# Kernel tuning notes

Hardware: AMD Instinct MI355X
Metric: run time of the kernel (lower is better)

The kernel has to match this reference:

```python
import jax, jax.numpy as jnp
import numpy as np

B, L, W, K, G = 8, 2048, 1024, 5, 2
OFFSET_SCALE = 2.0
EPS = 1e-5


def setup_inputs() -> dict:
    key = jax.random.key(0)
    ks = jax.random.split(key, 6)
    x = jax.random.normal(ks[0], (B, L, W), jnp.float32)
    # True = padded position
    lengths = jax.random.randint(ks[1], (B,), L // 2, L + 1)
    mask = jnp.arange(L)[None, :] >= lengths[:, None]
    # offset predictor (pointwise): one fractional offset per kernel tap
    w_off = jax.random.normal(ks[2], (W, K), jnp.float32) * 0.02
    b_off = jnp.zeros((K,), jnp.float32)
    # grouped conv weights: [groups, out_per_group, in_per_group, K]
    conv_w = jax.random.normal(ks[3], (G, W // G, W // G, K), jnp.float32) * 0.02
    conv_b = jnp.zeros((W,), jnp.float32)
    gamma = jnp.ones((W,), jnp.float32)
    beta = jnp.zeros((W,), jnp.float32)
    proj_w = jax.random.normal(ks[4], (W,), jnp.float32) * 0.02
    proj_b = jnp.zeros((), jnp.float32)
    return dict(x=x, mask=mask, w_off=w_off, b_off=b_off, conv_w=conv_w,
                conv_b=conv_b, gamma=gamma, beta=beta, proj_w=proj_w, proj_b=proj_b)


def _deform_conv1d(x, w_off, b_off, conv_w, conv_b):
    # x: [B, L, W]; returns [B, L, W]
    Bb, Ll, Ww = x.shape
    Gg, Co, Ci, Kk = conv_w.shape
    # per-position, per-tap fractional offsets in [-offset_scale, offset_scale]
    offsets = jnp.tanh(x @ w_off + b_off) * OFFSET_SCALE            # [B, L, K]
    taps = jnp.arange(Kk, dtype=x.dtype) - (Kk - 1) / 2.0           # centered taps
    pos = jnp.arange(Ll, dtype=x.dtype)[None, :, None] + taps[None, None, :] + offsets  # [B,L,K]
    p0 = jnp.floor(pos)
    frac = pos - p0                                                  # [B, L, K]
    p0i = p0.astype(jnp.int32)
    bidx = jnp.arange(Bb)[:, None, None]

    def gather(idx):
        valid = (idx >= 0) & (idx < Ll)                              # zero padding outside
        samp = x[bidx, jnp.clip(idx, 0, Ll - 1)]                     # [B, L, K, W]
        return samp * valid[..., None].astype(x.dtype)

    # linear interpolation between floor and floor+1 samples
    samp = gather(p0i) * (1.0 - frac)[..., None] + gather(p0i + 1) * frac[..., None]
    samp = samp.reshape(Bb, Ll, Kk, Gg, Ci)                          # split channels into groups
    out = jnp.einsum('blkgc,gock->blgo', samp, conv_w).reshape(Bb, Ll, Gg * Co)
    return out + conv_b


def reference(x, mask, w_off, b_off, conv_w, conv_b, gamma, beta, proj_w, proj_b):
    h = _deform_conv1d(x, w_off, b_off, conv_w, conv_b)              # [B, L, W]
    # LayerNorm over width
    mu = jnp.mean(h, axis=-1, keepdims=True)
    var = jnp.mean((h - mu) ** 2, axis=-1, keepdims=True)
    h = (h - mu) * jax.lax.rsqrt(var + EPS) * gamma + beta
    # dropout is identity in eval mode
    h = jnp.where(mask[..., None], 0.0, h)                           # masked fill
    lengths = jnp.maximum(jnp.sum(~mask, axis=1, keepdims=True).astype(h.dtype), 1.0)
    pooled = jnp.sum(h, axis=1) / lengths                            # [B, W]
    return pooled @ proj_w + proj_b                                  # [B]
```

## Files before the change

kernel.cpp:

```cpp
#include <hip/hip_runtime.h>
#include <hip/hip_bf16.h>

constexpr int Bb = 8, Ll = 2048, Ww = 1024;
constexpr int BL = Bb * Ll;

typedef short bf16x8 __attribute__((ext_vector_type(8)));
typedef float f32x4  __attribute__((ext_vector_type(4)));

__device__ inline unsigned short f2bf(float f) {
    union { float f; unsigned u; } v; v.f = f;
    unsigned u = v.u;
    unsigned r = (u + 0x7fffu + ((u >> 16) & 1u)) >> 16;
    return (unsigned short)r;
}
__device__ inline float bf2f(unsigned short h) {
    union { unsigned u; float f; } v; v.u = ((unsigned)h) << 16;
    return v.f;
}
__device__ inline unsigned lerp_pair(unsigned pa, unsigned pb, float w0, float w1) {
    union { unsigned u; float f; } alo, ahi, blo, bhi;
    alo.u = pa << 16;  ahi.u = pa & 0xffff0000u;
    blo.u = pb << 16;  bhi.u = pb & 0xffff0000u;
    float hlo = w0 * alo.f + w1 * blo.f;
    float hhi = w0 * ahi.f + w1 * bhi.f;
    union { __hip_bfloat162 h2; unsigned u; } r;
    r.h2 = __float22bfloat162_rn(float2{hlo, hhi});
    return r.u;
}

__device__ inline void gl_lds16(const unsigned short* g, unsigned short* l) {
    __builtin_amdgcn_global_load_lds(
        (const __attribute__((address_space(1))) unsigned int*)g,
        (__attribute__((address_space(3))) unsigned int*)l, 16, 0, 0);
}

__global__ void maskA_kernel(const void* __restrict__ mraw, int* __restrict__ flags) {
    const unsigned char* mb = (const unsigned char*)mraw;
    const unsigned* mw = (const unsigned*)mraw;
    int gid = blockIdx.x * 256 + threadIdx.x;
    int nonint = 0, notf = 0, hasf = 0;
    for (int i = gid; i < BL; i += 4096) { if ((i & 3) && mb[i]) nonint = 1; }
    for (int i = gid; i < BL / 4; i += 4096) {
        unsigned w = mw[i];
        if (w == 0x3f800000u) hasf = 1; else if (w) notf = 1;
    }
    if (__builtin_amdgcn_readfirstlane(__ballot(nonint) ? 1 : 0)) { if ((threadIdx.x & 63) == 0 && __ballot(nonint)) atomicOr(&flags[0], 1); }
    if ((threadIdx.x & 63) == 0) {
    }
    if (nonint) atomicOr(&flags[0], 1);
    if (notf)   atomicOr(&flags[1], 1);
    if (hasf)   atomicOr(&flags[2], 1);
}
__global__ void maskB_kernel(const void* __restrict__ mraw, const int* __restrict__ flags,
                             float* __restrict__ maskf) {
    const unsigned char* mb = (const unsigned char*)mraw;
    const unsigned* mw = (const unsigned*)mraw;
    int gid = blockIdx.x * 256 + threadIdx.x;
    int is_f32  = (!flags[1]) && flags[2];
    int is_bool = (!is_f32) && flags[0];
    for (int i = gid; i < BL; i += 4096) {
        int masked = is_bool ? (mb[i] != 0) : (mw[i] != 0u);
        maskf[i] = masked ? 0.0f : 1.0f;
    }
}

__global__ void wconv_kernel(const float* __restrict__ conv_w, unsigned short* __restrict__ w_t) {
    int gnt = blockIdx.x >> 2;
    int part = blockIdx.x & 3;
    int g = gnt / 20, nt = gnt % 20;
    int k = nt >> 2, o0 = (nt & 3) * 128;
    int tid = threadIdx.x;
    #pragma unroll
    for (int it = 0; it < 8; it++) {
        int chunk = part * 2048 + it * 256 + tid;
        int r = chunk >> 6;
        int cq = chunk & 63;
        int cs = cq >> 2, q = cq & 3;
        int o = o0 + r;
        int c0 = cs * 32 + q * 8;
        const float* src = conv_w + (((size_t)(g * 512 + o) * 512 + c0) * 5 + k);
        ushort4 lo, hi;
        lo.x = f2bf(src[0]);  lo.y = f2bf(src[5]);  lo.z = f2bf(src[10]); lo.w = f2bf(src[15]);
        hi.x = f2bf(src[20]); hi.y = f2bf(src[25]); hi.z = f2bf(src[30]); hi.w = f2bf(src[35]);
        int dst16 = (gnt * 16 + cs) * 512 + r * 4 + (q ^ (r & 3));
        *(ushort4*)&w_t[(size_t)dst16 * 8]     = lo;
        *(ushort4*)&w_t[(size_t)dst16 * 8 + 4] = hi;
    }
}

__global__ __launch_bounds__(256) void offsets_kernel(
    const float* __restrict__ x, const float* __restrict__ w_off, const float* __restrict__ b_off,
    unsigned short* __restrict__ x_bf, float4* __restrict__ pk)
{
    const int wave = threadIdx.x >> 6, lane = threadIdx.x & 63;
    const int bl = blockIdx.x * 4 + wave;
    const int l = bl & (Ll - 1);
    const int c0 = lane * 16;

    const float* xr = x + (size_t)bl * Ww + c0;
    float4 v0 = *(const float4*)(xr + 0);
    float4 v1 = *(const float4*)(xr + 4);
    float4 v2 = *(const float4*)(xr + 8);
    float4 v3 = *(const float4*)(xr + 12);
    float xv[16] = { v0.x,v0.y,v0.z,v0.w, v1.x,v1.y,v1.z,v1.w,
                     v2.x,v2.y,v2.z,v2.w, v3.x,v3.y,v3.z,v3.w };

    uint4 pa, pb;
    unsigned* pu = (unsigned*)&pa;
    #pragma unroll
    for (int j = 0; j < 4; j++) pu[j] = (unsigned)f2bf(xv[j*2]) | ((unsigned)f2bf(xv[j*2+1]) << 16);
    pu = (unsigned*)&pb;
    #pragma unroll
    for (int j = 0; j < 4; j++) pu[j] = (unsigned)f2bf(xv[8+j*2]) | ((unsigned)f2bf(xv[8+j*2+1]) << 16);
    *(uint4*)&x_bf[(size_t)bl * Ww + c0]     = pa;
    *(uint4*)&x_bf[(size_t)bl * Ww + c0 + 8] = pb;

    float acc[5] = {0.f, 0.f, 0.f, 0.f, 0.f};
    const float* wp = w_off + (size_t)c0 * 5;
    #pragma unroll
    for (int j = 0; j < 16; j++) {
        #pragma unroll
        for (int k = 0; k < 5; k++) acc[k] += xv[j] * wp[j * 5 + k];
    }
    #pragma unroll
    for (int k = 0; k < 5; k++)
        #pragma unroll
        for (int off = 32; off; off >>= 1) acc[k] += __shfl_xor(acc[k], off);

    if (lane < 5) {
        float s = (lane == 0) ? acc[0] : (lane == 1) ? acc[1] : (lane == 2) ? acc[2]
                : (lane == 3) ? acc[3] : acc[4];
        s += b_off[lane];
        float offv = tanhf(s) * 2.0f;
        float pos = (float)l + (float)(lane - 2) + offv;
        float p0 = floorf(pos);
        float frac = pos - p0;
        int i0 = (int)p0;
        int i1 = i0 + 1;
        int ok0 = (i0 >= 0) && (i0 < Ll);
        int ok1 = (i1 >= 0) && (i1 < Ll);
        float4 pkv;
        pkv.x = __int_as_float(min(max(i0, 0), Ll - 1));
        pkv.y = __int_as_float(min(max(i1, 0), Ll - 1));
        pkv.z = ok0 ? (1.0f - frac) : 0.0f;
        pkv.w = ok1 ? frac : 0.0f;
        pk[bl * 5 + lane] = pkv;
    }
}

__global__ __launch_bounds__(256, 2) void gemm_kernel(
    const unsigned short* __restrict__ x_bf, const unsigned short* __restrict__ w_t,
    const float4* __restrict__ pk, const float* __restrict__ conv_b,
    unsigned short* __restrict__ h)
{
    __shared__ unsigned short Bs[2][2 * 4096];
    const int tid = threadIdx.x;
    const int mt = blockIdx.x;
    const int nhalf = blockIdx.y;
    const int g = blockIdx.z;
    const int b = mt >> 4;
    const int lane = tid & 63, wave = tid >> 6;
    const int wr = (wave >> 1) * 64;
    const int imgsel = wave & 1;
    const int l15 = lane & 15, l4 = lane >> 4;
    const int sw = (l4 ^ (l15 & 3)) * 8;

    {
        const int nt0 = nhalf * 2;
        const unsigned short* W0 = w_t + ((size_t)((g * 20 + nt0) * 16 + 0)) * 4096;
        const unsigned short* W1 = w_t + ((size_t)((g * 20 + nt0 + 1) * 16 + 0)) * 4096;
        gl_lds16(W0 + tid * 8,        &Bs[0][tid * 8]);
        gl_lds16(W0 + 2048 + tid * 8, &Bs[0][2048 + tid * 8]);
        gl_lds16(W1 + tid * 8,        &Bs[0][4096 + tid * 8]);
        gl_lds16(W1 + 2048 + tid * 8, &Bs[0][4096 + 2048 + tid * 8]);
    }
    __syncthreads();

    f32x4 acc[4][8];
    #pragma unroll
    for (int i = 0; i < 4; i++)
        #pragma unroll
        for (int j = 0; j < 8; j++) acc[i][j] = (f32x4){0.f, 0.f, 0.f, 0.f};

    int buf = 0;
    for (int k = 0; k < 5; ++k) {
        unsigned off0[4], off1[4];
        float w0r[4], w1r[4];
        #pragma unroll
        for (int i = 0; i < 4; i++) {
            const int bl = mt * 128 + wr + i * 16 + l15;
            float4 pkv = pk[bl * 5 + k];
            const int i0 = __float_as_int(pkv.x), i1 = __float_as_int(pkv.y);
            off0[i] = (unsigned)(((b << 11) + i0) * Ww + g * 512);
            off1[i] = (unsigned)(((b << 11) + i1) * Ww + g * 512);
            w0r[i] = pkv.z; w1r[i] = pkv.w;
        }
        for (int cs = 0; cs < 16; ++cs) {
            const int it = k * 16 + cs;
            if (it < 79) {
                const int it2 = it + 1;
                const int k2 = it2 >> 4, cs2 = it2 & 15;
                const int nt0 = k2 * 4 + nhalf * 2;
                const unsigned short* W0 = w_t + ((size_t)((g * 20 + nt0) * 16 + cs2)) * 4096;
                const unsigned short* W1 = w_t + ((size_t)((g * 20 + nt0 + 1) * 16 + cs2)) * 4096;
                gl_lds16(W0 + tid * 8,        &Bs[buf ^ 1][tid * 8]);
                gl_lds16(W0 + 2048 + tid * 8, &Bs[buf ^ 1][2048 + tid * 8]);
                gl_lds16(W1 + tid * 8,        &Bs[buf ^ 1][4096 + tid * 8]);
                gl_lds16(W1 + 2048 + tid * 8, &Bs[buf ^ 1][4096 + 2048 + tid * 8]);
            }
            const int ch0 = cs * 32 + l4 * 8;
            bf16x8 af[4];
            #pragma unroll
            for (int i = 0; i < 4; i++) {
                const uint4 ua = *(const uint4*)(x_bf + off0[i] + ch0);
                const uint4 ub = *(const uint4*)(x_bf + off1[i] + ch0);
                union { unsigned u[4]; bf16x8 v; } fa;
                fa.u[0] = lerp_pair(ua.x, ub.x, w0r[i], w1r[i]);
                fa.u[1] = lerp_pair(ua.y, ub.y, w0r[i], w1r[i]);
                fa.u[2] = lerp_pair(ua.z, ub.z, w0r[i], w1r[i]);
                fa.u[3] = lerp_pair(ua.w, ub.w, w0r[i], w1r[i]);
                af[i] = fa.v;
            }
            bf16x8 bfr[8];
            #pragma unroll
            for (int j = 0; j < 8; j++)
                bfr[j] = *(const bf16x8*)&Bs[buf][imgsel * 4096 + (j * 16 + l15) * 32 + sw];
            #pragma unroll
            for (int i = 0; i < 4; i++)
                #pragma unroll
                for (int j = 0; j < 8; j++)
                    acc[i][j] = __builtin_amdgcn_mfma_f32_16x16x32_bf16(af[i], bfr[j], acc[i][j], 0, 0, 0);
            __syncthreads();
            buf ^= 1;
        }
    }
    #pragma unroll
    for (int j = 0; j < 8; j++) {
        const int col = g * 512 + nhalf * 256 + imgsel * 128 + j * 16 + l15;
        const float bias = conv_b[col];
        #pragma unroll
        for (int i = 0; i < 4; i++) {
            const int row0 = mt * 128 + wr + i * 16 + l4 * 4;
            #pragma unroll
            for (int rr = 0; rr < 4; rr++)
                h[(size_t)(row0 + rr) * Ww + col] = f2bf(acc[i][j][rr] + bias);
        }
    }
}

__global__ __launch_bounds__(256) void lnpool_kernel(
    const unsigned short* __restrict__ h, const float* __restrict__ gamma,
    const float* __restrict__ maskf, float* __restrict__ pooled)
{
    const int tid = threadIdx.x;
    const int wave = tid >> 6, lane = tid & 63;
    const int c0 = lane * 16;
    const int bl0 = blockIdx.x * 16 + wave * 4;
    const int b = bl0 >> 11;

    float g16[16];
    #pragma unroll
    for (int j = 0; j < 4; j++) {
        float4 gv = *(const float4*)(gamma + c0 + j * 4);
        g16[j*4+0] = gv.x; g16[j*4+1] = gv.y; g16[j*4+2] = gv.z; g16[j*4+3] = gv.w;
    }
    float pacc[16];
    #pragma unroll
    for (int j = 0; j < 16; j++) pacc[j] = 0.f;

    #pragma unroll
    for (int r = 0; r < 4; r++) {
        const int bl = bl0 + r;
        const float m = maskf[bl];
        const uint4 ha = *(const uint4*)(h + (size_t)bl * Ww + c0);
        const uint4 hb = *(const uint4*)(h + (size_t)bl * Ww + c0 + 8);
        float hf[16];
        const unsigned* pw = (const unsigned*)&ha;
        #pragma unroll
        for (int j = 0; j < 4; j++) {
            union { unsigned u; float f; } lo, hi;
            lo.u = pw[j] << 16; hi.u = pw[j] & 0xffff0000u;
            hf[j*2] = lo.f; hf[j*2+1] = hi.f;
        }
        pw = (const unsigned*)&hb;
        #pragma unroll
        for (int j = 0; j < 4; j++) {
            union { unsigned u; float f; } lo, hi;
            lo.u = pw[j] << 16; hi.u = pw[j] & 0xffff0000u;
            hf[8+j*2] = lo.f; hf[8+j*2+1] = hi.f;
        }
        float s1 = 0.f, s2 = 0.f;
        #pragma unroll
        for (int j = 0; j < 16; j++) { s1 += hf[j]; s2 += hf[j] * hf[j]; }
        #pragma unroll
        for (int off = 32; off; off >>= 1) {
            s1 += __shfl_xor(s1, off);
            s2 += __shfl_xor(s2, off);
        }
        const float mu = s1 * (1.0f / 1024.0f);
        const float var = s2 * (1.0f / 1024.0f) - mu * mu;
        const float rstd = rsqrtf(var + 1e-5f) * m;
        #pragma unroll
        for (int j = 0; j < 16; j++) pacc[j] += (hf[j] - mu) * rstd * g16[j];
    }
    __shared__ float spool[4][1024];
    #pragma unroll
    for (int j = 0; j < 4; j++)
        *(float4*)&spool[wave][c0 + j * 4] = *(float4*)&pacc[j * 4];
    __syncthreads();
    const int ch = tid * 4;
    float4 a = *(float4*)&spool[0][ch];
    float4 bq = *(float4*)&spool[1][ch];
    float4 cq = *(float4*)&spool[2][ch];
    float4 dq = *(float4*)&spool[3][ch];
    atomicAdd(&pooled[b * Ww + ch + 0], a.x + bq.x + cq.x + dq.x);
    atomicAdd(&pooled[b * Ww + ch + 1], a.y + bq.y + cq.y + dq.y);
    atomicAdd(&pooled[b * Ww + ch + 2], a.z + bq.z + cq.z + dq.z);
    atomicAdd(&pooled[b * Ww + ch + 3], a.w + bq.w + cq.w + dq.w);
}

__global__ void final_kernel(const float* __restrict__ pooled, const float* __restrict__ maskf,
                             const float* __restrict__ beta, const float* __restrict__ proj_w,
                             const float* __restrict__ proj_b, float* __restrict__ out)
{
    int b = blockIdx.x;
    int tid = threadIdx.x;
    float len = 0.f, dotP = 0.f, dotB = 0.f;
    for (int l = tid; l < Ll; l += 256) len += maskf[b * Ll + l];
    for (int c = tid; c < Ww; c += 256) {
        dotP += pooled[b * Ww + c] * proj_w[c];
        dotB += beta[c] * proj_w[c];
    }
    for (int off = 32; off; off >>= 1) {
        len += __shfl_down(len, off);
        dotP += __shfl_down(dotP, off);
        dotB += __shfl_down(dotB, off);
    }
    __shared__ float rl[4], rp[4], rb[4];
    int wave = tid >> 6, lane = tid & 63;
    if (lane == 0) { rl[wave] = len; rp[wave] = dotP; rb[wave] = dotB; }
    __syncthreads();
    if (tid == 0) {
        float Lt = rl[0] + rl[1] + rl[2] + rl[3];
        float Pt = rp[0] + rp[1] + rp[2] + rp[3];
        float Bt = rb[0] + rb[1] + rb[2] + rb[3];
        out[b] = Pt / fmaxf(Lt, 1.0f) + Bt + proj_b[0];
    }
}


extern "C" void kernel_launch(void* const* d_in, const int* in_sizes, int n_in,
                              void* d_out, int out_size, void* d_ws, size_t ws_size,
                              hipStream_t stream)
{
    const float* x      = (const float*)d_in[0];
    const void*  mask   = d_in[1];
    const float* w_off  = (const float*)d_in[2];
    const float* b_off  = (const float*)d_in[3];
    const float* conv_w = (const float*)d_in[4];
    const float* conv_b = (const float*)d_in[5];
    const float* gamma  = (const float*)d_in[6];
    const float* beta   = (const float*)d_in[7];
    const float* proj_w = (const float*)d_in[8];
    const float* proj_b = (const float*)d_in[9];
    float* out = (float*)d_out;

    char* ws = (char*)d_ws;
    float* maskf         = (float*)(ws + 0);
    float* pooled        = (float*)(ws + 65536);
    int*   flags         = (int*)(ws + 98304);
    float4* pk           = (float4*)(ws + 98320);
    unsigned short* w_t  = (unsigned short*)(ws + 1409040);
    unsigned short* x_bf = (unsigned short*)(ws + 6651920);
    unsigned short* h    = (unsigned short*)(ws + 40206352);

    hipMemsetAsync(pooled, 0, Bb * Ww * sizeof(float), stream);
    hipMemsetAsync(flags, 0, 16, stream);
    maskA_kernel<<<16, 256, 0, stream>>>(mask, flags);
    maskB_kernel<<<16, 256, 0, stream>>>(mask, flags, maskf);
    wconv_kernel<<<160, 256, 0, stream>>>(conv_w, w_t);
    offsets_kernel<<<BL / 4, 256, 0, stream>>>(x, w_off, b_off, x_bf, pk);
    gemm_kernel<<<dim3(128, 2, 2), 256, 0, stream>>>(x_bf, w_t, pk, conv_b, h);
    lnpool_kernel<<<1024, 256, 0, stream>>>(h, gamma, maskf, pooled);
    final_kernel<<<8, 256, 0, stream>>>(pooled, maskf, beta, proj_w, proj_b, out);
}
```

Before: 353.7 us.

## Fuse prep kernels into one launch, halve GEMM M-tile, fold mask into lnpool

Merges the mask-detection, weight-conversion and offset kernels into a single prep_kernel dispatched by block index, and drops the separate maskB pass. The mask value is now decoded inside lnpool, which also accumulates per-batch lengths with atomics, so final_kernel no longer rescans the mask. The GEMM M tile shrinks from 128 to 64 rows with a doubled grid and launch bounds raised to 4 waves per SIMD, trading operand reuse for more blocks and occupancy. The launch count drops, and there are more atomics plus lower per-block reuse in the GEMM.

Measured after the change: 392.5 us. 1.11x slower.

```diff
diff --git a/kernel.cpp b/kernel.cpp
--- a/kernel.cpp
+++ b/kernel.cpp
@@ -34,121 +34,108 @@
         (__attribute__((address_space(3))) unsigned int*)l, 16, 0, 0);
 }
 
-__global__ void maskA_kernel(const void* __restrict__ mraw, int* __restrict__ flags) {
-    const unsigned char* mb = (const unsigned char*)mraw;
-    const unsigned* mw = (const unsigned*)mraw;
-    int gid = blockIdx.x * 256 + threadIdx.x;
-    int nonint = 0, notf = 0, hasf = 0;
-    for (int i = gid; i < BL; i += 4096) { if ((i & 3) && mb[i]) nonint = 1; }
-    for (int i = gid; i < BL / 4; i += 4096) {
-        unsigned w = mw[i];
-        if (w == 0x3f800000u) hasf = 1; else if (w) notf = 1;
-    }
-    if (__builtin_amdgcn_readfirstlane(__ballot(nonint) ? 1 : 0)) { if ((threadIdx.x & 63) == 0 && __ballot(nonint)) atomicOr(&flags[0], 1); }
-    if ((threadIdx.x & 63) == 0) {
-    }
-    if (nonint) atomicOr(&flags[0], 1);
-    if (notf)   atomicOr(&flags[1], 1);
-    if (hasf)   atomicOr(&flags[2], 1);
-}
-__global__ void maskB_kernel(const void* __restrict__ mraw, const int* __restrict__ flags,
-                             float* __restrict__ maskf) {
-    const unsigned char* mb = (const unsigned char*)mraw;
-    const unsigned* mw = (const unsigned*)mraw;
-    int gid = blockIdx.x * 256 + threadIdx.x;
-    int is_f32  = (!flags[1]) && flags[2];
-    int is_bool = (!is_f32) && flags[0];
-    for (int i = gid; i < BL; i += 4096) {
-        int masked = is_bool ? (mb[i] != 0) : (mw[i] != 0u);
-        maskf[i] = masked ? 0.0f : 1.0f;
-    }
-}
-
-__global__ void wconv_kernel(const float* __restrict__ conv_w, unsigned short* __restrict__ w_t) {
-    int gnt = blockIdx.x >> 2;
-    int part = blockIdx.x & 3;
-    int g = gnt / 20, nt = gnt % 20;
-    int k = nt >> 2, o0 = (nt & 3) * 128;
-    int tid = threadIdx.x;
-    #pragma unroll
-    for (int it = 0; it < 8; it++) {
-        int chunk = part * 2048 + it * 256 + tid;
-        int r = chunk >> 6;
-        int cq = chunk & 63;
-        int cs = cq >> 2, q = cq & 3;
-        int o = o0 + r;
-        int c0 = cs * 32 + q * 8;
-        const float* src = conv_w + (((size_t)(g * 512 + o) * 512 + c0) * 5 + k);
-        ushort4 lo, hi;
-        lo.x = f2bf(src[0]);  lo.y = f2bf(src[5]);  lo.z = f2bf(src[10]); lo.w = f2bf(src[15]);
-        hi.x = f2bf(src[20]); hi.y = f2bf(src[25]); hi.z = f2bf(src[30]); hi.w = f2bf(src[35]);
-        int dst16 = (gnt * 16 + cs) * 512 + r * 4 + (q ^ (r & 3));
-        *(ushort4*)&w_t[(size_t)dst16 * 8]     = lo;
-        *(ushort4*)&w_t[(size_t)dst16 * 8 + 4] = hi;
-    }
-}
-
-__global__ __launch_bounds__(256) void offsets_kernel(
+__global__ __launch_bounds__(256) void prep_kernel(
     const float* __restrict__ x, const float* __restrict__ w_off, const float* __restrict__ b_off,
-    unsigned short* __restrict__ x_bf, float4* __restrict__ pk)
-{
-    const int wave = threadIdx.x >> 6, lane = threadIdx.x & 63;
-    const int bl = blockIdx.x * 4 + wave;
-    const int l = bl & (Ll - 1);
-    const int c0 = lane * 16;
-
-    const float* xr = x + (size_t)bl * Ww + c0;
-    float4 v0 = *(const float4*)(xr + 0);
-    float4 v1 = *(const float4*)(xr + 4);
-    float4 v2 = *(const float4*)(xr + 8);
-    float4 v3 = *(const float4*)(xr + 12);
-    float xv[16] = { v0.x,v0.y,v0.z,v0.w, v1.x,v1.y,v1.z,v1.w,
-                     v2.x,v2.y,v2.z,v2.w, v3.x,v3.y,v3.z,v3.w };
-
-    uint4 pa, pb;
-    unsigned* pu = (unsigned*)&pa;
-    #pragma unroll
-    for (int j = 0; j < 4; j++) pu[j] = (unsigned)f2bf(xv[j*2]) | ((unsigned)f2bf(xv[j*2+1]) << 16);
-    pu = (unsigned*)&pb;
-    #pragma unroll
-    for (int j = 0; j < 4; j++) pu[j] = (unsigned)f2bf(xv[8+j*2]) | ((unsigned)f2bf(xv[8+j*2+1]) << 16);
-    *(uint4*)&x_bf[(size_t)bl * Ww + c0]     = pa;
-    *(uint4*)&x_bf[(size_t)bl * Ww + c0 + 8] = pb;
-
-    float acc[5] = {0.f, 0.f, 0.f, 0.f, 0.f};
-    const float* wp = w_off + (size_t)c0 * 5;
-    #pragma unroll
-    for (int j = 0; j < 16; j++) {
-        #pragma unroll
-        for (int k = 0; k < 5; k++) acc[k] += xv[j] * wp[j * 5 + k];
-    }
-    #pragma unroll
-    for (int k = 0; k < 5; k++)
-        #pragma unroll
-        for (int off = 32; off; off >>= 1) acc[k] += __shfl_xor(acc[k], off);
-
-    if (lane < 5) {
-        float s = (lane == 0) ? acc[0] : (lane == 1) ? acc[1] : (lane == 2) ? acc[2]
-                : (lane == 3) ? acc[3] : acc[4];
-        s += b_off[lane];
-        float offv = tanhf(s) * 2.0f;
-        float pos = (float)l + (float)(lane - 2) + offv;
-        float p0 = floorf(pos);
-        float frac = pos - p0;
-        int i0 = (int)p0;
-        int i1 = i0 + 1;
-        int ok0 = (i0 >= 0) && (i0 < Ll);
-        int ok1 = (i1 >= 0) && (i1 < Ll);
-        float4 pkv;
-        pkv.x = __int_as_float(min(max(i0, 0), Ll - 1));
-        pkv.y = __int_as_float(min(max(i1, 0), Ll - 1));
-        pkv.z = ok0 ? (1.0f - frac) : 0.0f;
-        pkv.w = ok1 ? frac : 0.0f;
-        pk[bl * 5 + lane] = pkv;
-    }
-}
-
-__global__ __launch_bounds__(256, 2) void gemm_kernel(
+    const float* __restrict__ conv_w, const void* __restrict__ mraw,
+    unsigned short* __restrict__ x_bf, float4* __restrict__ pk,
+    unsigned short* __restrict__ w_t, int* __restrict__ flags)
+{
+    const int blk = blockIdx.x;
+    const int tid = threadIdx.x;
+    if (blk < 4096) {
+        const int wave = tid >> 6, lane = tid & 63;
+        const int bl = blk * 4 + wave;
+        const int l = bl & (Ll - 1);
+        const int c0 = lane * 16;
+
+        const float* xr = x + (size_t)bl * Ww + c0;
+        float4 v0 = *(const float4*)(xr + 0);
+        float4 v1 = *(const float4*)(xr + 4);
+        float4 v2 = *(const float4*)(xr + 8);
+        float4 v3 = *(const float4*)(xr + 12);
+        float xv[16] = { v0.x,v0.y,v0.z,v0.w, v1.x,v1.y,v1.z,v1.w,
+                         v2.x,v2.y,v2.z,v2.w, v3.x,v3.y,v3.z,v3.w };
+
+        uint4 pa, pb;
+        unsigned* pu = (unsigned*)&pa;
+        #pragma unroll
+        for (int j = 0; j < 4; j++) pu[j] = (unsigned)f2bf(xv[j*2]) | ((unsigned)f2bf(xv[j*2+1]) << 16);
+        pu = (unsigned*)&pb;
+        #pragma unroll
+        for (int j = 0; j < 4; j++) pu[j] = (unsigned)f2bf(xv[8+j*2]) | ((unsigned)f2bf(xv[8+j*2+1]) << 16);
+        *(uint4*)&x_bf[(size_t)bl * Ww + c0]     = pa;
+        *(uint4*)&x_bf[(size_t)bl * Ww + c0 + 8] = pb;
+
+        float acc[5] = {0.f, 0.f, 0.f, 0.f, 0.f};
+        const float* wp = w_off + (size_t)c0 * 5;
+        #pragma unroll
+        for (int j = 0; j < 16; j++) {
+            #pragma unroll
+            for (int k = 0; k < 5; k++) acc[k] += xv[j] * wp[j * 5 + k];
+        }
+        #pragma unroll
+        for (int k = 0; k < 5; k++)
+            #pragma unroll
+            for (int off = 32; off; off >>= 1) acc[k] += __shfl_xor(acc[k], off);
+
+        if (lane < 5) {
+            float s = (lane == 0) ? acc[0] : (lane == 1) ? acc[1] : (lane == 2) ? acc[2]
+                    : (lane == 3) ? acc[3] : acc[4];
+            s += b_off[lane];
+            float offv = tanhf(s) * 2.0f;
+            float pos = (float)l + (float)(lane - 2) + offv;
+            float p0 = floorf(pos);
+            float frac = pos - p0;
+            int i0 = (int)p0;
+            int i1 = i0 + 1;
+            int ok0 = (i0 >= 0) && (i0 < Ll);
+            int ok1 = (i1 >= 0) && (i1 < Ll);
+            float4 pkv;
+            pkv.x = __int_as_float(min(max(i0, 0), Ll - 1));
+            pkv.y = __int_as_float(min(max(i1, 0), Ll - 1));
+            pkv.z = ok0 ? (1.0f - frac) : 0.0f;
+            pkv.w = ok1 ? frac : 0.0f;
+            pk[bl * 5 + lane] = pkv;
+        }
+    } else if (blk < 4256) {
+        const int bb = blk - 4096;
+        const int gnt = bb >> 2;
+        const int part = bb & 3;
+        const int g = gnt / 20, nt = gnt % 20;
+        const int k = nt >> 2, o0 = (nt & 3) * 128;
+        #pragma unroll
+        for (int it = 0; it < 8; it++) {
+            int chunk = part * 2048 + it * 256 + tid;
+            int r = chunk >> 6;
+            int cq = chunk & 63;
+            int cs = cq >> 2, q = cq & 3;
+            int o = o0 + r;
+            int c0 = cs * 32 + q * 8;
+            const float* src = conv_w + (((size_t)(g * 512 + o) * 512 + c0) * 5 + k);
+            ushort4 lo, hi;
+            lo.x = f2bf(src[0]);  lo.y = f2bf(src[5]);  lo.z = f2bf(src[10]); lo.w = f2bf(src[15]);
+            hi.x = f2bf(src[20]); hi.y = f2bf(src[25]); hi.z = f2bf(src[30]); hi.w = f2bf(src[35]);
+            int dst16 = (gnt * 16 + cs) * 512 + r * 4 + (q ^ (r & 3));
+            *(ushort4*)&w_t[(size_t)dst16 * 8]     = lo;
+            *(ushort4*)&w_t[(size_t)dst16 * 8 + 4] = hi;
+        }
+    } else {
+        const unsigned char* mb = (const unsigned char*)mraw;
+        const unsigned* mw = (const unsigned*)mraw;
+        int gid = (blk - 4256) * 256 + tid;
+        int nonint = 0, notf = 0, hasf = 0;
+        for (int i = gid; i < BL; i += 4096) { if ((i & 3) && mb[i]) nonint = 1; }
+        for (int i = gid; i < BL / 4; i += 4096) {
+            unsigned w = mw[i];
+            if (w == 0x3f800000u) hasf = 1; else if (w) notf = 1;
+        }
+        if (nonint) atomicOr(&flags[0], 1);
+        if (notf)   atomicOr(&flags[1], 1);
+        if (hasf)   atomicOr(&flags[2], 1);
+    }
+}
+
+__global__ __launch_bounds__(256, 4) void gemm_kernel(
     const unsigned short* __restrict__ x_bf, const unsigned short* __restrict__ w_t,
     const float4* __restrict__ pk, const float* __restrict__ conv_b,
     unsigned short* __restrict__ h)
@@ -158,9 +145,9 @@
     const int mt = blockIdx.x;
     const int nhalf = blockIdx.y;
     const int g = blockIdx.z;
-    const int b = mt >> 4;
+    const int b = mt >> 5;
     const int lane = tid & 63, wave = tid >> 6;
-    const int wr = (wave >> 1) * 64;
+    const int wr = (wave >> 1) * 32;
     const int imgsel = wave & 1;
     const int l15 = lane & 15, l4 = lane >> 4;
     const int sw = (l4 ^ (l15 & 3)) * 8;
@@ -176,19 +163,19 @@
     }
     __syncthreads();
 
-    f32x4 acc[4][8];
-    #pragma unroll
-    for (int i = 0; i < 4; i++)
+    f32x4 acc[2][8];
+    #pragma unroll
+    for (int i = 0; i < 2; i++)
         #pragma unroll
         for (int j = 0; j < 8; j++) acc[i][j] = (f32x4){0.f, 0.f, 0.f, 0.f};
 
     int buf = 0;
     for (int k = 0; k < 5; ++k) {
-        unsigned off0[4], off1[4];
-        float w0r[4], w1r[4];
-        #pragma unroll
-        for (int i = 0; i < 4; i++) {
-            const int bl = mt * 128 + wr + i * 16 + l15;
+        unsigned off0[2], off1[2];
+        float w0r[2], w1r[2];
+        #pragma unroll
+        for (int i = 0; i < 2; i++) {
+            const int bl = mt * 64 + wr + i * 16 + l15;
             float4 pkv = pk[bl * 5 + k];
             const int i0 = __float_as_int(pkv.x), i1 = __float_as_int(pkv.y);
             off0[i] = (unsigned)(((b << 11) + i0) * Ww + g * 512);
@@ -209,9 +196,9 @@
                 gl_lds16(W1 + 2048 + tid * 8, &Bs[buf ^ 1][4096 + 2048 + tid * 8]);
             }
             const int ch0 = cs * 32 + l4 * 8;
-            bf16x8 af[4];
-            #pragma unroll
-            for (int i = 0; i < 4; i++) {
+            bf16x8 af[2];
+            #pragma unroll
+            for (int i = 0; i < 2; i++) {
                 const uint4 ua = *(const uint4*)(x_bf + off0[i] + ch0);
                 const uint4 ub = *(const uint4*)(x_bf + off1[i] + ch0);
                 union { unsigned u[4]; bf16x8 v; } fa;
@@ -226,7 +213,7 @@
             for (int j = 0; j < 8; j++)
                 bfr[j] = *(const bf16x8*)&Bs[buf][imgsel * 4096 + (j * 16 + l15) * 32 + sw];
             #pragma unroll
-            for (int i = 0; i < 4; i++)
+            for (int i = 0; i < 2; i++)
                 #pragma unroll
                 for (int j = 0; j < 8; j++)
                     acc[i][j] = __builtin_amdgcn_mfma_f32_16x16x32_bf16(af[i], bfr[j], acc[i][j], 0, 0, 0);
@@ -239,8 +226,8 @@
         const int col = g * 512 + nhalf * 256 + imgsel * 128 + j * 16 + l15;
         const float bias = conv_b[col];
         #pragma unroll
-        for (int i = 0; i < 4; i++) {
-            const int row0 = mt * 128 + wr + i * 16 + l4 * 4;
+        for (int i = 0; i < 2; i++) {
+            const int row0 = mt * 64 + wr + i * 16 + l4 * 4;
             #pragma unroll
             for (int rr = 0; rr < 4; rr++)
                 h[(size_t)(row0 + rr) * Ww + col] = f2bf(acc[i][j][rr] + bias);
@@ -250,7 +237,8 @@
 
 __global__ __launch_bounds__(256) void lnpool_kernel(
     const unsigned short* __restrict__ h, const float* __restrict__ gamma,
-    const float* __restrict__ maskf, float* __restrict__ pooled)
+    const void* __restrict__ mraw, const int* __restrict__ flags,
+    float* __restrict__ pooled, float* __restrict__ lengths)
 {
     const int tid = threadIdx.x;
     const int wave = tid >> 6, lane = tid & 63;
@@ -258,6 +246,11 @@
     const int bl0 = blockIdx.x * 16 + wave * 4;
     const int b = bl0 >> 11;
 
+    const unsigned char* mb = (const unsigned char*)mraw;
+    const unsigned* mw = (const unsigned*)mraw;
+    const int is_f32  = (!flags[1]) && flags[2];
+    const int is_bool = (!is_f32) && flags[0];
+
     float g16[16];
     #pragma unroll
     for (int j = 0; j < 4; j++) {
@@ -267,11 +260,14 @@
     float pacc[16];
     #pragma unroll
     for (int j = 0; j < 16; j++) pacc[j] = 0.f;
+    float cnt = 0.f;
 
     #pragma unroll
     for (int r = 0; r < 4; r++) {
         const int bl = bl0 + r;
-        const float m = maskf[bl];
+        const int masked = is_bool ? (mb[bl] != 0) : (mw[bl] != 0u);
+        const float m = masked ? 0.0f : 1.0f;
+        cnt += m;
         const uint4 ha = *(const uint4*)(h + (size_t)bl * Ww + c0);
         const uint4 hb = *(const uint4*)(h + (size_t)bl * Ww + c0 + 8);
         float hf[16];
@@ -303,6 +299,7 @@
         #pragma unroll
         for (int j = 0; j < 16; j++) pacc[j] += (hf[j] - mu) * rstd * g16[j];
     }
+    if (lane == 0) atomicAdd(&lengths[b], cnt);
     __shared__ float spool[4][1024];
     #pragma unroll
     for (int j = 0; j < 4; j++)
@@ -319,32 +316,29 @@
     atomicAdd(&pooled[b * Ww + ch + 3], a.w + bq.w + cq.w + dq.w);
 }
 
-__global__ void final_kernel(const float* __restrict__ pooled, const float* __restrict__ maskf,
+__global__ void final_kernel(const float* __restrict__ pooled, const float* __restrict__ lengths,
                              const float* __restrict__ beta, const float* __restrict__ proj_w,
                              const float* __restrict__ proj_b, float* __restrict__ out)
 {
     int b = blockIdx.x;
     int tid = threadIdx.x;
-    float len = 0.f, dotP = 0.f, dotB = 0.f;
-    for (int l = tid; l < Ll; l += 256) len += maskf[b * Ll + l];
+    float dotP = 0.f, dotB = 0.f;
     for (int c = tid; c < Ww; c += 256) {
         dotP += pooled[b * Ww + c] * proj_w[c];
         dotB += beta[c] * proj_w[c];
     }
     for (int off = 32; off; off >>= 1) {
-        len += __shfl_down(len, off);
         dotP += __shfl_down(dotP, off);
         dotB += __shfl_down(dotB, off);
     }
-    __shared__ float rl[4], rp[4], rb[4];
+    __shared__ float rp[4], rb[4];
     int wave = tid >> 6, lane = tid & 63;
-    if (lane == 0) { rl[wave] = len; rp[wave] = dotP; rb[wave] = dotB; }
+    if (lane == 0) { rp[wave] = dotP; rb[wave] = dotB; }
     __syncthreads();
     if (tid == 0) {
-        float Lt = rl[0] + rl[1] + rl[2] + rl[3];
         float Pt = rp[0] + rp[1] + rp[2] + rp[3];
         float Bt = rb[0] + rb[1] + rb[2] + rb[3];
-        out[b] = Pt / fmaxf(Lt, 1.0f) + Bt + proj_b[0];
+        out[b] = Pt / fmaxf(lengths[b], 1.0f) + Bt + proj_b[0];
     }
 }
 
@@ -366,21 +360,17 @@
     float* out = (float*)d_out;
 
     char* ws = (char*)d_ws;
-    float* maskf         = (float*)(ws + 0);
-    float* pooled        = (float*)(ws + 65536);
-    int*   flags         = (int*)(ws + 98304);
-    float4* pk           = (float4*)(ws + 98320);
-    unsigned short* w_t  = (unsigned short*)(ws + 1409040);
-    unsigned short* x_bf = (unsigned short*)(ws + 6651920);
-    unsigned short* h    = (unsigned short*)(ws + 40206352);
-
-    hipMemsetAsync(pooled, 0, Bb * Ww * sizeof(float), stream);
-    hipMemsetAsync(flags, 0, 16, stream);
-    maskA_kernel<<<16, 256, 0, stream>>>(mask, flags);
-    maskB_kernel<<<16, 256, 0, stream>>>(mask, flags, maskf);
-    wconv_kernel<<<160, 256, 0, stream>>>(conv_w, w_t);
-    offsets_kernel<<<BL / 4, 256, 0, stream>>>(x, w_off, b_off, x_bf, pk);
-    gemm_kernel<<<dim3(128, 2, 2), 256, 0, stream>>>(x_bf, w_t, pk, conv_b, h);
-    lnpool_kernel<<<1024, 256, 0, stream>>>(h, gamma, maskf, pooled);
-    final_kernel<<<8, 256, 0, stream>>>(pooled, maskf, beta, proj_w, proj_b, out);
-}
+    float* pooled        = (float*)(ws + 0);
+    int*   flags         = (int*)(ws + 32768);
+    float* lengths       = (float*)(ws + 32784);
+    float4* pk           = (float4*)(ws + 32832);
+    unsigned short* w_t  = (unsigned short*)(ws + 1343552);
+    unsigned short* x_bf = (unsigned short*)(ws + 6586432);
+    unsigned short* h    = (unsigned short*)(ws + 40140864);
+
+    hipMemsetAsync(pooled, 0, 32832, stream);
+    prep_kernel<<<4272, 256, 0, stream>>>(x, w_off, b_off, conv_w, mask, x_bf, pk, w_t, flags);
+    gemm_kernel<<<dim3(256, 2, 2), 256, 0, stream>>>(x_bf, w_t, pk, conv_b, h);
+    lnpool_kernel<<<1024, 256, 0, stream>>>(h, gamma, mask, flags, pooled, lengths);
+    final_kernel<<<8, 256, 0, stream>>>(pooled, lengths, beta, proj_w, proj_b, out);
+}
```
